# Optimization experiments

Measured on AMD Instinct MI355X. Metric: run time of the kernel, lower is better.

The kernel has to match this reference:

```python
import jax, jax.numpy as jnp
import numpy as np

N = 50000
E = 1600000
IN_C = 128
HID_C = 128
OUT_C = 64
NUM_REL = 8
NUM_BASES = 4


def rgcn_conv(x, edge_index, edge_type, basis, comp, root, bias):
    """Faithful PyG RGCNConv with basis decomposition and mean aggregation.

    basis: (num_bases, in, out); comp: (num_rel, num_bases);
    root: (in, out); bias: (out,).
    """
    # Compose per-relation weights from bases: W_r = sum_b comp[r,b] * basis[b]
    W = jnp.einsum('rb,bio->rio', comp, basis)  # (R, in, out)
    src, dst = edge_index[0], edge_index[1]
    # Segment id encodes (relation, dst node) so one segment_sum handles all relations
    seg = edge_type * N + dst  # (E,)
    msgs = x[src]  # (E, in) gather
    sums = jax.ops.segment_sum(msgs, seg, num_segments=NUM_REL * N)
    cnt = jax.ops.segment_sum(jnp.ones((seg.shape[0],), dtype=x.dtype), seg,
                              num_segments=NUM_REL * N)
    mean = sums / jnp.maximum(cnt, 1.0)[:, None]  # mean aggr; empty segs -> 0
    agg = mean.reshape(NUM_REL, N, -1)  # (R, N, in)
    out = jnp.einsum('rni,rio->no', agg, W)
    out = out + x @ root + bias  # root/self-loop weight + bias
    return out


def setup_inputs() -> dict:
    key = jax.random.key(0)
    ks = jax.random.split(key, 12)
    x = jax.random.normal(ks[0], (N, IN_C), dtype=jnp.float32)
    A = jax.random.randint(ks[1], (2, E), 0, N, dtype=jnp.int64)
    edge_type = jax.random.randint(ks[2], (E,), 0, NUM_REL, dtype=jnp.int64)
    def glorot(k, shape):
        fan_in, fan_out = shape[-2], shape[-1]
        lim = jnp.sqrt(6.0 / (fan_in + fan_out)).astype(jnp.float32)
        return jax.random.uniform(k, shape, jnp.float32, -lim, lim)
    w1_basis = glorot(ks[3], (NUM_BASES, IN_C, HID_C))
    w1_comp = glorot(ks[4], (NUM_REL, NUM_BASES))
    w1_root = glorot(ks[5], (IN_C, HID_C))
    w1_bias = jnp.zeros((HID_C,), jnp.float32)
    w2_basis = glorot(ks[6], (NUM_BASES, HID_C, OUT_C))
    w2_comp = glorot(ks[7], (NUM_REL, NUM_BASES))
    w2_root = glorot(ks[8], (HID_C, OUT_C))
    w2_bias = jnp.zeros((OUT_C,), jnp.float32)
    return {"x": x, "A": A, "edge_type": edge_type,
            "w1_basis": w1_basis, "w1_comp": w1_comp, "w1_root": w1_root, "w1_bias": w1_bias,
            "w2_basis": w2_basis, "w2_comp": w2_comp, "w2_root": w2_root, "w2_bias": w2_bias}


def reference(x, A, edge_type, w1_basis, w1_comp, w1_root, w1_bias,
              w2_basis, w2_comp, w2_root, w2_bias):
    h = rgcn_conv(x, A, edge_type, w1_basis, w1_comp, w1_root, w1_bias)
    h = jax.nn.relu(h)
    out = rgcn_conv(h, A, edge_type, w2_basis, w2_comp, w2_root, w2_bias)
    return out
```

## Files before the change

kernel.cpp:

```cpp
#include <hip/hip_runtime.h>


#define N_NODES 50000
#define N_EDGES 1600000
#define N_REL   8
#define CAP     32

typedef __attribute__((ext_vector_type(8))) short short8;
typedef __attribute__((ext_vector_type(4))) float f32x4;

__device__ __forceinline__ ushort f2bf(float x) {
    unsigned u = __builtin_bit_cast(unsigned, x);
    u += 0x7FFFu + ((u >> 16) & 1u);
    return (ushort)(u >> 16);
}
__device__ __forceinline__ float u2f(unsigned u) {
    return __builtin_bit_cast(float, u);
}

__global__ void zero_i32_kernel(int* __restrict__ p, int n) {
    int i = blockIdx.x * 256 + threadIdx.x;
    if (i < n) p[i] = 0;
}

__global__ void to_bf16_kernel(const float* __restrict__ in,
                               ushort* __restrict__ out) {
    int i = blockIdx.x * 256 + threadIdx.x;
    int total = (N_NODES + 1) * 16;
    if (i >= total) return;
    int base = i * 8;
    short8 v;
    if (base < N_NODES * 128) {
        f32x4 a = *(const f32x4*)(in + base);
        f32x4 b = *(const f32x4*)(in + base + 4);
        v = (short8){(short)f2bf(a.x), (short)f2bf(a.y), (short)f2bf(a.z),
                     (short)f2bf(a.w), (short)f2bf(b.x), (short)f2bf(b.y),
                     (short)f2bf(b.z), (short)f2bf(b.w)};
    } else {
        v = (short8){0, 0, 0, 0, 0, 0, 0, 0};
    }
    *(short8*)(out + base) = v;
}

__global__ void compose_wt_kernel(const float* __restrict__ basis,
                                  const float* __restrict__ comp,
                                  const float* __restrict__ root,
                                  ushort* __restrict__ Wt,
                                  int outc, int total) {
    int i = blockIdx.x * 256 + threadIdx.x;
    if (i >= total) return;
    int per_r = outc << 7;
    int r = i / per_r;
    int rem = i - r * per_r;
    int n = rem >> 7;
    int k = rem & 127;
    float s;
    if (r == N_REL) {
        s = root[k * outc + n];
    } else {
        s = 0.f;
#pragma unroll
        for (int b = 0; b < 4; ++b)
            s += comp[r * 4 + b] * basis[(b * 128 + k) * outc + n];
    }
    Wt[i] = f2bf(s);
}

__global__ void build_ell_kernel(const int* __restrict__ A,
                                 const int* __restrict__ etype,
                                 int* __restrict__ cnt,
                                 ushort* __restrict__ ell) {
    int e = blockIdx.x * 256 + threadIdx.x;
    if (e >= N_EDGES) return;
    int s = A[e];
    int d = A[N_EDGES + e];
    int t = etype[e];
    int seg = t * N_NODES + d;
    int slot = atomicAdd(&cnt[seg], 1);
    if (slot < CAP) ell[(size_t)seg * CAP + slot] = (ushort)s;
}

template <int OUTC, bool RELU, bool BF16OUT>
__global__ __launch_bounds__(256, 8)
void rgcn_layer_mfma(const ushort* __restrict__ xbf,
                     const int* __restrict__ cnt,
                     const ushort* __restrict__ ell,
                     const ushort* __restrict__ Wt,
                     const float* __restrict__ bias,
                     void* __restrict__ outp) {
    constexpr int LDK = 136;
    constexpr int TN  = 32;
    constexpr int NCH = OUTC / 32;

    __shared__ ushort meanT[TN * LDK];
    __shared__ ushort Wl[32 * LDK];

    const int tid   = threadIdx.x;
    const int lane  = tid & 63;
    const int wave  = tid >> 6;
    const int nbase = blockIdx.x * TN;

    const int g  = tid >> 4;
    const int j  = tid & 15;
    const int j8 = j * 8;
    const int gb = lane & 48;

    const int rt = wave & 1;
    const int ch = wave >> 1;
    const int lr = lane & 15;
    const int kc = (lane >> 4) * 8;

    f32x4 acc[NCH];
#pragma unroll
    for (int t = 0; t < NCH; ++t) acc[t] = (f32x4){0.f, 0.f, 0.f, 0.f};

    for (int r = 0; r <= N_REL; ++r) {
#pragma unroll
        for (int p = 0; p < 2; ++p) {
            int a  = p * 16 + g;
            int gn = nbase + a;
            short8 sv = (short8){0, 0, 0, 0, 0, 0, 0, 0};
            if (gn < N_NODES) {
                if (r == N_REL) {
                    sv = *(const short8*)(xbf + (size_t)gn * 128 + j8);
                } else {
                    int seg = r * N_NODES + gn;
                    int c   = cnt[seg];
                    int cc  = c < CAP ? c : CAP;
                    uint pre = *(const uint*)(ell + (size_t)seg * CAP + 2 * j);
                    f32x4 s0 = (f32x4){0.f, 0.f, 0.f, 0.f};
                    f32x4 s1 = (f32x4){0.f, 0.f, 0.f, 0.f};
                    int ccr = (cc + 3) & ~3;
                    for (int e = 0; e < ccr; e += 4) {
                        uint ua = __shfl(pre, gb + (e >> 1), 64);
                        uint ub = __shfl(pre, gb + (e >> 1) + 1, 64);
                        int i0 = (e + 0 < cc) ? (int)(ua & 0xFFFFu) : N_NODES;
                        int i1 = (e + 1 < cc) ? (int)(ua >> 16)     : N_NODES;
                        int i2 = (e + 2 < cc) ? (int)(ub & 0xFFFFu) : N_NODES;
                        int i3 = (e + 3 < cc) ? (int)(ub >> 16)     : N_NODES;
                        short8 v0 = *(const short8*)(xbf + (size_t)i0 * 128 + j8);
                        short8 v1 = *(const short8*)(xbf + (size_t)i1 * 128 + j8);
                        short8 v2 = *(const short8*)(xbf + (size_t)i2 * 128 + j8);
                        short8 v3 = *(const short8*)(xbf + (size_t)i3 * 128 + j8);
#pragma unroll
                        for (int u = 0; u < 4; ++u) {
                            short8 v = (u == 0) ? v0 : (u == 1) ? v1
                                     : (u == 2) ? v2 : v3;
                            uint4 w = __builtin_bit_cast(uint4, v);
                            s0.x += u2f(w.x << 16);
                            s0.y += u2f(w.x & 0xFFFF0000u);
                            s0.z += u2f(w.y << 16);
                            s0.w += u2f(w.y & 0xFFFF0000u);
                            s1.x += u2f(w.z << 16);
                            s1.y += u2f(w.z & 0xFFFF0000u);
                            s1.z += u2f(w.w << 16);
                            s1.w += u2f(w.w & 0xFFFF0000u);
                        }
                    }
                    float inv = 1.f / (float)(c > 1 ? c : 1);
                    s0 *= inv;
                    s1 *= inv;
                    sv = (short8){(short)f2bf(s0.x), (short)f2bf(s0.y),
                                  (short)f2bf(s0.z), (short)f2bf(s0.w),
                                  (short)f2bf(s1.x), (short)f2bf(s1.y),
                                  (short)f2bf(s1.z), (short)f2bf(s1.w)};
                }
            }
            *(short8*)&meanT[a * LDK + j8] = sv;
        }
        __syncthreads();

        short8 af[4];
        const int m = rt * 16 + lr;
#pragma unroll
        for (int ks = 0; ks < 4; ++ks)
            af[ks] = *(const short8*)&meanT[m * LDK + ks * 32 + kc];

#pragma unroll
        for (int c = 0; c < NCH; ++c) {
            {
                const float4* src =
                    (const float4*)(Wt + ((size_t)r * OUTC + c * 32) * 128);
#pragma unroll
                for (int q = 0; q < 2; ++q) {
                    int idx = tid + q * 256;
                    int n   = idx >> 4;
                    int k8  = idx & 15;
                    *(float4*)&Wl[n * LDK + k8 * 8] = src[idx];
                }
            }
            __syncthreads();
            const int n = ch * 16 + lr;
            f32x4 a = acc[c];
#pragma unroll
            for (int ks = 0; ks < 4; ++ks) {
                short8 bf = *(const short8*)&Wl[n * LDK + ks * 32 + kc];
                a = __builtin_amdgcn_mfma_f32_16x16x32_bf16(af[ks], bf, a,
                                                            0, 0, 0);
            }
            acc[c] = a;
            if (c + 1 < NCH) __syncthreads();
        }
    }

    const int rq = (lane >> 4) * 4;
#pragma unroll
    for (int t = 0; t < NCH; ++t) {
        int col  = t * 32 + ch * 16 + lr;
        float bv = bias[col];
#pragma unroll
        for (int q = 0; q < 4; ++q) {
            int node = nbase + rt * 16 + rq + q;
            if (node < N_NODES) {
                float v = acc[t][q] + bv;
                if (RELU) v = fmaxf(v, 0.f);
                if (BF16OUT)
                    ((ushort*)outp)[(size_t)node * OUTC + col] = f2bf(v);
                else
                    ((float*)outp)[(size_t)node * OUTC + col] = v;
            }
        }
    }
}

extern "C" void kernel_launch(void* const* d_in, const int* in_sizes, int n_in,
                              void* d_out, int out_size, void* d_ws, size_t ws_size,
                              hipStream_t stream) {
    const float* x        = (const float*)d_in[0];
    const int*   A        = (const int*)d_in[1];
    const int*   etype    = (const int*)d_in[2];
    const float* w1_basis = (const float*)d_in[3];
    const float* w1_comp  = (const float*)d_in[4];
    const float* w1_root  = (const float*)d_in[5];
    const float* w1_bias  = (const float*)d_in[6];
    const float* w2_basis = (const float*)d_in[7];
    const float* w2_comp  = (const float*)d_in[8];
    const float* w2_root  = (const float*)d_in[9];
    const float* w2_bias  = (const float*)d_in[10];
    float* out = (float*)d_out;

    char* ws = (char*)d_ws;
    ushort* Wt1  = (ushort*)(ws);
    ushort* Wt2  = (ushort*)(ws + (512 << 10));
    int*    cnt  = (int*)(ws + (1 << 20));
    ushort* x_bf = (ushort*)(ws + (3ull << 20));
    ushort* h_bf = (ushort*)(ws + (16ull << 20));
    ushort* ell  = (ushort*)(ws + (29ull << 20));

    zero_i32_kernel<<<(N_REL * N_NODES + 255) / 256, 256, 0, stream>>>(
        cnt, N_REL * N_NODES);
    to_bf16_kernel<<<((N_NODES + 1) * 16 + 255) / 256, 256, 0, stream>>>(x, x_bf);
    zero_i32_kernel<<<1, 64, 0, stream>>>((int*)(h_bf + (size_t)N_NODES * 128), 64);
    compose_wt_kernel<<<(9 * 128 * 128 + 255) / 256, 256, 0, stream>>>(
        w1_basis, w1_comp, w1_root, Wt1, 128, 9 * 128 * 128);
    compose_wt_kernel<<<(9 * 64 * 128 + 255) / 256, 256, 0, stream>>>(
        w2_basis, w2_comp, w2_root, Wt2, 64, 9 * 64 * 128);
    build_ell_kernel<<<(N_EDGES + 255) / 256, 256, 0, stream>>>(A, etype, cnt, ell);

    int grid = (N_NODES + 31) / 32;
    rgcn_layer_mfma<128, true, true><<<grid, 256, 0, stream>>>(
        x_bf, cnt, ell, Wt1, w1_bias, h_bf);
    rgcn_layer_mfma<64, false, false><<<grid, 256, 0, stream>>>(
        h_bf, cnt, ell, Wt2, w2_bias, out);
}
```

Before: 386.7 us.

## Replace fixed-capacity ELL adjacency with compact padded CSR built via histogram and scan

Replaces the single-pass ELL build (fixed 32 slots per segment) with three passes: a histogram of counts, a wave-level prefix scan that assigns offsets padded to multiples of 4, and a fill pass that scatters source ids into a compact CSR array. The layer kernels read offset and count packed together from one int2. Output stores become nontemporal. The aim is to cut the neighbour-list footprint and improve its cache locality, at the cost of two extra kernel launches and a second atomic pass over the edges. Offsets are handed out per wave through a global atomic, so segment order in memory is not deterministic. Segments with more than 32 edges are still truncated when read.

```diff
diff --git a/kernel.cpp b/kernel.cpp
--- a/kernel.cpp
+++ b/kernel.cpp
@@ -5,6 +5,7 @@
 #define N_EDGES 1600000
 #define N_REL   8
 #define CAP     32
+#define NSEG    (N_REL * N_NODES)
 
 typedef __attribute__((ext_vector_type(8))) short short8;
 typedef __attribute__((ext_vector_type(4))) float f32x4;
@@ -66,25 +67,57 @@
     Wt[i] = f2bf(s);
 }
 
-__global__ void build_ell_kernel(const int* __restrict__ A,
-                                 const int* __restrict__ etype,
-                                 int* __restrict__ cnt,
-                                 ushort* __restrict__ ell) {
+__global__ void hist_kernel(const int* __restrict__ A,
+                            const int* __restrict__ et,
+                            int* __restrict__ cnt) {
     int e = blockIdx.x * 256 + threadIdx.x;
     if (e >= N_EDGES) return;
-    int s = A[e];
-    int d = A[N_EDGES + e];
-    int t = etype[e];
+    int d = __builtin_nontemporal_load(A + N_EDGES + e);
+    int t = __builtin_nontemporal_load(et + e);
+    atomicAdd(&cnt[t * N_NODES + d], 1);
+}
+
+__global__ void off_kernel(const int* __restrict__ cnt,
+                           int2* __restrict__ packed,
+                           int* __restrict__ gcur) {
+    int s = blockIdx.x * 256 + threadIdx.x;
+    int lane = threadIdx.x & 63;
+    int c = (s < NSEG) ? cnt[s] : 0;
+    int need = (c + 3) & ~3;
+    int pre = need;
+#pragma unroll
+    for (int o = 1; o < 64; o <<= 1) {
+        int v = __shfl_up(pre, o, 64);
+        if (lane >= o) pre += v;
+    }
+    int total = __shfl(pre, 63, 64);
+    int base = 0;
+    if (lane == 63) base = atomicAdd(gcur, total);
+    base = __shfl(base, 63, 64);
+    if (s < NSEG) packed[s] = make_int2(base + pre - need, c);
+}
+
+__global__ void fill_kernel(const int* __restrict__ A,
+                            const int* __restrict__ et,
+                            const int2* __restrict__ packed,
+                            int* __restrict__ wcnt,
+                            ushort* __restrict__ csr) {
+    int e = blockIdx.x * 256 + threadIdx.x;
+    if (e >= N_EDGES) return;
+    int sv = __builtin_nontemporal_load(A + e);
+    int d  = __builtin_nontemporal_load(A + N_EDGES + e);
+    int t  = __builtin_nontemporal_load(et + e);
     int seg = t * N_NODES + d;
-    int slot = atomicAdd(&cnt[seg], 1);
-    if (slot < CAP) ell[(size_t)seg * CAP + slot] = (ushort)s;
+    int slot = atomicAdd(&wcnt[seg], 1);
+    int off = packed[seg].x;
+    csr[(size_t)off + slot] = (ushort)sv;
 }
 
 template <int OUTC, bool RELU, bool BF16OUT>
 __global__ __launch_bounds__(256, 8)
 void rgcn_layer_mfma(const ushort* __restrict__ xbf,
-                     const int* __restrict__ cnt,
-                     const ushort* __restrict__ ell,
+                     const int2* __restrict__ packed,
+                     const ushort* __restrict__ csr,
                      const ushort* __restrict__ Wt,
                      const float* __restrict__ bias,
                      void* __restrict__ outp) {
@@ -125,9 +158,10 @@
                     sv = *(const short8*)(xbf + (size_t)gn * 128 + j8);
                 } else {
                     int seg = r * N_NODES + gn;
-                    int c   = cnt[seg];
+                    int2 oc = packed[seg];
+                    int c   = oc.y;
                     int cc  = c < CAP ? c : CAP;
-                    uint pre = *(const uint*)(ell + (size_t)seg * CAP + 2 * j);
+                    uint pre = *(const uint*)(csr + (size_t)oc.x + 2 * j);
                     f32x4 s0 = (f32x4){0.f, 0.f, 0.f, 0.f};
                     f32x4 s1 = (f32x4){0.f, 0.f, 0.f, 0.f};
                     int ccr = (cc + 3) & ~3;
@@ -215,9 +249,11 @@
                 float v = acc[t][q] + bv;
                 if (RELU) v = fmaxf(v, 0.f);
                 if (BF16OUT)
-                    ((ushort*)outp)[(size_t)node * OUTC + col] = f2bf(v);
+                    __builtin_nontemporal_store(
+                        f2bf(v), (ushort*)outp + (size_t)node * OUTC + col);
                 else
-                    ((float*)outp)[(size_t)node * OUTC + col] = v;
+                    __builtin_nontemporal_store(
+                        v, (float*)outp + (size_t)node * OUTC + col);
             }
         }
     }
@@ -243,23 +279,30 @@
     ushort* Wt1  = (ushort*)(ws);
     ushort* Wt2  = (ushort*)(ws + (512 << 10));
     int*    cnt  = (int*)(ws + (1 << 20));
-    ushort* x_bf = (ushort*)(ws + (3ull << 20));
-    ushort* h_bf = (ushort*)(ws + (16ull << 20));
-    ushort* ell  = (ushort*)(ws + (29ull << 20));
-
-    zero_i32_kernel<<<(N_REL * N_NODES + 255) / 256, 256, 0, stream>>>(
-        cnt, N_REL * N_NODES);
+    int*    wcnt = cnt + NSEG;
+    int*    gcur = wcnt + NSEG;
+    ushort* x_bf = (ushort*)(ws + (5ull << 20));
+    ushort* h_bf = (ushort*)(ws + (18ull << 20));
+    int2*   packed = (int2*)(ws + (31ull << 20));
+    ushort* csr  = (ushort*)(ws + (35ull << 20));
+
+    zero_i32_kernel<<<(2 * NSEG + 1 + 255) / 256, 256, 0, stream>>>(
+        cnt, 2 * NSEG + 1);
     to_bf16_kernel<<<((N_NODES + 1) * 16 + 255) / 256, 256, 0, stream>>>(x, x_bf);
     zero_i32_kernel<<<1, 64, 0, stream>>>((int*)(h_bf + (size_t)N_NODES * 128), 64);
     compose_wt_kernel<<<(9 * 128 * 128 + 255) / 256, 256, 0, stream>>>(
         w1_basis, w1_comp, w1_root, Wt1, 128, 9 * 128 * 128);
     compose_wt_kernel<<<(9 * 64 * 128 + 255) / 256, 256, 0, stream>>>(
         w2_basis, w2_comp, w2_root, Wt2, 64, 9 * 64 * 128);
-    build_ell_kernel<<<(N_EDGES + 255) / 256, 256, 0, stream>>>(A, etype, cnt, ell);
+
+    hist_kernel<<<(N_EDGES + 255) / 256, 256, 0, stream>>>(A, etype, cnt);
+    off_kernel<<<(NSEG + 255) / 256, 256, 0, stream>>>(cnt, packed, gcur);
+    fill_kernel<<<(N_EDGES + 255) / 256, 256, 0, stream>>>(
+        A, etype, packed, wcnt, csr);
 
     int grid = (N_NODES + 31) / 32;
     rgcn_layer_mfma<128, true, true><<<grid, 256, 0, stream>>>(
-        x_bf, cnt, ell, Wt1, w1_bias, h_bf);
+        x_bf, packed, csr, Wt1, w1_bias, h_bf);
     rgcn_layer_mfma<64, false, false><<<grid, 256, 0, stream>>>(
-        h_bf, cnt, ell, Wt2, w2_bias, out);
-}
+        h_bf, packed, csr, Wt2, w2_bias, out);
+}
```

Measured after the change: 495.1 us. +28.0%, slower.
